# Optimization experiments

Hardware: AMD Instinct MI355X
Metric: run time of the kernel (lower is better)

## Reference

```python
import jax, jax.numpy as jnp
import numpy as np

EPS = 1e-8
TEMP3 = 10.0


def setup_inputs() -> dict:
    key = jax.random.key(0)
    k1, k2, k3 = jax.random.split(key, 3)
    B, D = 8192, 512
    cnn_code = jax.random.normal(k1, (B, D), dtype=jnp.float32)
    rnn_code = jax.random.normal(k2, (B, D), dtype=jnp.float32)
    idx = jax.random.uniform(k3, (B, B), dtype=jnp.float32)
    # ensure every row has at least one positive (> threshold1=0.8), as the
    # original divides by len(pos)
    diag = jnp.arange(B)
    idx = idx.at[diag, diag].set(0.95)
    probs = jnp.array([0.8, 0.5], dtype=jnp.float32)  # (threshold1, threshold2)
    return {"cnn_code": cnn_code, "rnn_code": rnn_code, "idx": idx, "probs": probs}


def reference(cnn_code, rnn_code, idx, probs):
    B = cnn_code.shape[0]
    fdt = cnn_code.dtype
    # cosine similarity * temp3  -> scores0 [B,B]
    cn = jnp.linalg.norm(cnn_code, axis=-1, keepdims=True)   # [B,1]
    rn = jnp.linalg.norm(rnn_code, axis=-1, keepdims=True)   # [B,1]
    scores0 = (cnn_code @ rnn_code.T) / jnp.clip(cn * rn.T, EPS) * TEMP3
    scores1 = scores0.T

    th1, th2 = probs[0], probs[1]
    pos_mask = idx > th1    # [B,B] ragged positive sets per row
    neg_mask = idx <= th2   # [B,B] ragged negative sets per row
    n_pos = pos_mask.sum(axis=1).astype(fdt)          # [B]
    n_neg = neg_mask.sum(axis=1).astype(fdt)          # [B]

    neginf = jnp.array(-jnp.inf, dtype=fdt)
    # logsumexp over each row's negative set (shared across all positives j)
    lse_neg0 = jax.nn.logsumexp(jnp.where(neg_mask, scores0, neginf), axis=1)  # [B]
    lse_neg1 = jax.nn.logsumexp(jnp.where(neg_mask, scores1, neginf), axis=1)  # [B]

    # For each positive j: logits = concat([score_j, neg_scores]); target puts
    # mass 1 on index 0; softXEnt divides by logits length (1 + n_neg).
    denom = (1.0 + n_neg)[:, None]                                            # [B,1]
    l0 = -(scores0 - jnp.logaddexp(scores0, lse_neg0[:, None])) / denom       # [B,B]
    l1 = -(scores1 - jnp.logaddexp(scores1, lse_neg1[:, None])) / denom

    loss0 = (jnp.where(pos_mask, l0, 0.0).sum(axis=1) / n_pos).sum() / B
    loss1 = (jnp.where(pos_mask, l1, 0.0).sum(axis=1) / n_pos).sum() / B
    return loss0 + loss1
```

## Files before the change

kernel.cpp:

```cpp
#include <hip/hip_runtime.h>
#include <hip/hip_bf16.h>
#include <math.h>
#include <stdint.h>

#define BDIM 8192
#define DDIM 512
#define NT   64
#define BK   64
#define TEMP 10.0f
#define PLW  128

typedef __attribute__((ext_vector_type(8))) short bf16x8;
typedef __attribute__((ext_vector_type(4))) float f32x4;
typedef unsigned long long u64;
typedef unsigned int u32;

__device__ __forceinline__ unsigned short f2bf(float f) {
  unsigned int x = __float_as_uint(f);
  x += 0x7fffu + ((x >> 16) & 1u);
  return (unsigned short)(x >> 16);
}

__device__ __forceinline__ void gld16(const void* gptr, void* lptr) {
  __builtin_amdgcn_global_load_lds((const __attribute__((address_space(1))) u32*)gptr,
                                   (__attribute__((address_space(3))) u32*)lptr, 16, 0, 0);
}

__device__ __forceinline__ float red16_dpp(float x) {
  x += __int_as_float(__builtin_amdgcn_mov_dpp(__float_as_int(x), 0xB1, 0xF, 0xF, true));
  x += __int_as_float(__builtin_amdgcn_mov_dpp(__float_as_int(x), 0x4E, 0xF, 0xF, true));
  x += __int_as_float(__builtin_amdgcn_mov_dpp(__float_as_int(x), 0x141, 0xF, 0xF, true));
  x += __int_as_float(__builtin_amdgcn_mov_dpp(__float_as_int(x), 0x140, 0xF, 0xF, true));
  return x;
}

__global__ __launch_bounds__(256) void knorm(const float* __restrict__ cnn,
                                             const float* __restrict__ rnn,
                                             unsigned short* __restrict__ u,
                                             unsigned short* __restrict__ v) {
  int wid = threadIdx.x >> 6, lane = threadIdx.x & 63;
  int gw = blockIdx.x * 4 + wid;
  const float* src;
  unsigned short* dst;
  int row;
  float mul;
  if (gw < BDIM) { src = cnn; dst = u; row = gw; mul = TEMP; }
  else           { src = rnn; dst = v; row = gw - BDIM; mul = 1.0f; }
  const float* p = src + (size_t)row * DDIM + lane * 8;
  float4 a0 = *(const float4*)p;
  float4 a1 = *(const float4*)(p + 4);
  float ss = a0.x*a0.x + a0.y*a0.y + a0.z*a0.z + a0.w*a0.w
           + a1.x*a1.x + a1.y*a1.y + a1.z*a1.z + a1.w*a1.w;
#pragma unroll
  for (int m = 1; m <= 32; m <<= 1) ss += __shfl_xor(ss, m);
  float inv = mul / sqrtf(ss);
  unsigned short o[8];
  o[0] = f2bf(a0.x * inv); o[1] = f2bf(a0.y * inv);
  o[2] = f2bf(a0.z * inv); o[3] = f2bf(a0.w * inv);
  o[4] = f2bf(a1.x * inv); o[5] = f2bf(a1.y * inv);
  o[6] = f2bf(a1.z * inv); o[7] = f2bf(a1.w * inv);
  *(uint4*)(dst + (size_t)row * DDIM + lane * 8) = *(uint4*)o;
}

__global__ __launch_bounds__(256) void kmask(const float* __restrict__ idx,
                                             const float* __restrict__ probs,
                                             unsigned char* __restrict__ posb,
                                             unsigned char* __restrict__ negb,
                                             float* __restrict__ npr,
                                             float* __restrict__ nnr) {
  const float th1 = probs[0], th2 = probs[1];
  int wid = threadIdx.x >> 6, lane = threadIdx.x & 63;
  int row = blockIdx.x * 4 + wid;
  const float4* src = (const float4*)(idx + (size_t)row * BDIM);
  unsigned char* pr = posb + (size_t)row * 1024;
  unsigned char* nr = negb + (size_t)row * 1024;
  int np = 0, nn = 0;
#pragma unroll 2
  for (int i = 0; i < 16; i++) {
    float4 x0 = src[i * 128 + lane * 2];
    float4 x1 = src[i * 128 + lane * 2 + 1];
    float xs[8] = {x0.x, x0.y, x0.z, x0.w, x1.x, x1.y, x1.z, x1.w};
    unsigned pb = 0, nb = 0;
#pragma unroll
    for (int k = 0; k < 8; k++) {
      pb |= (xs[k] > th1 ? 1u : 0u) << k;
      nb |= (xs[k] <= th2 ? 1u : 0u) << k;
    }
    pr[i * 64 + lane] = (unsigned char)pb;
    nr[i * 64 + lane] = (unsigned char)nb;
    np += __popc(pb); nn += __popc(nb);
  }
#pragma unroll
  for (int m = 1; m <= 32; m <<= 1) {
    np += __shfl_xor(np, m);
    nn += __shfl_xor(nn, m);
  }
  if (lane == 0) { npr[row] = (float)np; nnr[row] = (float)nn; }
}

__global__ __launch_bounds__(256, 3) void kmain(const unsigned short* __restrict__ u,
                                                const unsigned short* __restrict__ v,
                                                const u64* __restrict__ posp,
                                                const u64* __restrict__ negp,
                                                float* __restrict__ P) {
  __shared__ unsigned short aT[128 * BK];
  __shared__ unsigned short bT[128 * BK];
  __shared__ float L0[3 * 128];
  __shared__ float L1[3 * 128];
  const int tid = threadIdx.x, lane = tid & 63, wid = tid >> 6;
  const int l15 = lane & 15, lg = lane >> 4;
  const int qr = wid >> 1, qc = wid & 1;

  for (int t = tid; t < 768; t += 256) {
    if (t < 384) L0[t] = 0.f; else L1[t - 384] = 0.f;
  }

  const int bid = blockIdx.x;
  const int xcd = bid & 7, n = bid >> 3;
  const int st = n >> 6, w = n & 63;
  const int ti = xcd * 8 + (w & 7);
  const int tj = st * 8 + (w >> 3);
  const int I = ti * 128, J = tj * 128;

  f32x4 acc[4][4];
#pragma unroll
  for (int a = 0; a < 4; a++)
#pragma unroll
    for (int b = 0; b < 4; b++) acc[a][b] = (f32x4){0, 0, 0, 0};

  const unsigned short* gA = u + (size_t)(I + wid * 32 + (lane >> 3)) * DDIM + (lane & 7) * 8;
  const unsigned short* gB = v + (size_t)(J + wid * 32 + (lane >> 3)) * DDIM + (lane & 7) * 8;
  unsigned short* lA = aT + (wid * 32 + (lane >> 3)) * BK + (lane & 7) * 8;
  unsigned short* lB = bT + (wid * 32 + (lane >> 3)) * BK + (lane & 7) * 8;

  for (int k0 = 0; k0 < DDIM; k0 += BK) {
#pragma unroll
    for (int c = 0; c < 4; c++) {
      gld16(gA + (size_t)c * 8 * DDIM + k0, lA + c * 8 * BK);
      gld16(gB + (size_t)c * 8 * DDIM + k0, lB + c * 8 * BK);
    }
    __syncthreads();
#pragma unroll
    for (int kk = 0; kk < 2; kk++) {
      bf16x8 af[4], bf_[4];
#pragma unroll
      for (int ar = 0; ar < 4; ar++)
        af[ar] = *(const bf16x8*)(aT + (qr * 64 + ar * 16 + l15) * BK + kk * 32 + lg * 8);
#pragma unroll
      for (int bc = 0; bc < 4; bc++)
        bf_[bc] = *(const bf16x8*)(bT + (qc * 64 + bc * 16 + l15) * BK + kk * 32 + lg * 8);
#pragma unroll
      for (int ar = 0; ar < 4; ar++)
#pragma unroll
        for (int bc = 0; bc < 4; bc++)
          acc[ar][bc] = __builtin_amdgcn_mfma_f32_16x16x32_bf16(af[ar], bf_[bc], acc[ar][bc], 0, 0, 0);
    }
    __syncthreads();
  }

  u64 pw1[4], nw1[4];
#pragma unroll
  for (int bc = 0; bc < 4; bc++) {
    size_t w1 = (size_t)(J + qc * 64 + bc * 16 + l15) * PLW + (I >> 6) + qr;
    pw1[bc] = posp[w1] >> (lg * 4);
    nw1[bc] = negp[w1] >> (lg * 4);
  }

  float zn1[4] = {0, 0, 0, 0}, zp1[4] = {0, 0, 0, 0}, sm1[4] = {0, 0, 0, 0};

#pragma unroll
  for (int ar = 0; ar < 4; ar++) {
    u64 pw[4], nw[4];
#pragma unroll
    for (int j = 0; j < 4; j++) {
      int R = qr * 64 + ar * 16 + lg * 4 + j;
      size_t w0 = (size_t)(I + R) * PLW + (J >> 6) + qc;
      pw[j] = posp[w0] >> l15;
      nw[j] = negp[w0] >> l15;
    }
#pragma unroll
    for (int j = 0; j < 4; j++) {
      float zn0 = 0, zp0 = 0, sm0 = 0;
#pragma unroll
      for (int bc = 0; bc < 4; bc++) {
        float s = acc[ar][bc][j];
        float e = __expf(s - TEMP);
        float mp0 = (float)((unsigned)(pw[j]  >> (bc * 16)) & 1u);
        float mn0 = (float)((unsigned)(nw[j]  >> (bc * 16)) & 1u);
        float mp1 = (float)((unsigned)(pw1[bc] >> (ar * 16 + j)) & 1u);
        float mn1 = (float)((unsigned)(nw1[bc] >> (ar * 16 + j)) & 1u);
        zp0 = fmaf(mp0, e, zp0);
        sm0 = fmaf(mp0, s, sm0);
        zn0 = fmaf(mn0, e, zn0);
        zp1[bc] = fmaf(mp1, e, zp1[bc]);
        sm1[bc] = fmaf(mp1, s, sm1[bc]);
        zn1[bc] = fmaf(mn1, e, zn1[bc]);
      }
      zn0 = red16_dpp(zn0); zp0 = red16_dpp(zp0); sm0 = red16_dpp(sm0);
      if (l15 == 0) {
        int R = qr * 64 + ar * 16 + lg * 4 + j;
        atomicAdd(&L0[0 * 128 + R], zn0);
        atomicAdd(&L0[1 * 128 + R], zp0);
        atomicAdd(&L0[2 * 128 + R], sm0);
      }
    }
  }

#pragma unroll
  for (int bc = 0; bc < 4; bc++) {
    float zn = zn1[bc], zp = zp1[bc], sm = sm1[bc];
    zn += __shfl_xor(zn, 16); zn += __shfl_xor(zn, 32);
    zp += __shfl_xor(zp, 16); zp += __shfl_xor(zp, 32);
    sm += __shfl_xor(sm, 16); sm += __shfl_xor(sm, 32);
    if (lg == 0) {
      int C = qc * 64 + bc * 16 + l15;
      atomicAdd(&L1[0 * 128 + C], zn);
      atomicAdd(&L1[1 * 128 + C], zp);
      atomicAdd(&L1[2 * 128 + C], sm);
    }
  }
  __syncthreads();

  for (int t = tid; t < 768; t += 256) {
    int s = t >> 7, c = t & 127;
    if (s < 3) P[((size_t)tj * 6 + s) * BDIM + I + c] = L0[s * 128 + c];
    else       P[((size_t)ti * 6 + s) * BDIM + J + c] = L1[(s - 3) * 128 + c];
  }
}

__global__ __launch_bounds__(128) void kfinal(const float* __restrict__ P,
                                              const float* __restrict__ npr,
                                              const float* __restrict__ nnr,
                                              float* __restrict__ part) {
  int r = blockIdx.x * 128 + threadIdx.x;
  float st[6] = {0, 0, 0, 0, 0, 0};
  for (int k = 0; k < 64; k++) {
#pragma unroll
    for (int s = 0; s < 6; s++) st[s] += P[((size_t)k * 6 + s) * BDIM + r];
  }
  float np = npr[r], nn = nnr[r];
  float inv = 1.f / (np * (1.f + nn));
  float l0 = (np * (TEMP + logf(st[0])) - st[2] + st[1] / st[0]) * inv;
  float l1 = (np * (TEMP + logf(st[3])) - st[5] + st[4] / st[3]) * inv;
  float tot = l0 + l1;
#pragma unroll
  for (int m = 1; m <= 32; m <<= 1) tot += __shfl_xor(tot, m);
  __shared__ float sb;
  if (threadIdx.x == 0) sb = tot;
  __syncthreads();
  if (threadIdx.x == 64) part[blockIdx.x] = sb + tot;
}

__global__ __launch_bounds__(64) void kfinal2(const float* __restrict__ part,
                                              float* __restrict__ out) {
  float t = part[threadIdx.x];
#pragma unroll
  for (int m = 1; m <= 32; m <<= 1) t += __shfl_xor(t, m);
  if (threadIdx.x == 0) out[0] = t / (float)BDIM;
}

extern "C" void kernel_launch(void* const* d_in, const int* in_sizes, int n_in,
                              void* d_out, int out_size, void* d_ws, size_t ws_size,
                              hipStream_t stream) {
  (void)in_sizes; (void)n_in; (void)out_size; (void)ws_size;
  const float* cnn   = (const float*)d_in[0];
  const float* rnn   = (const float*)d_in[1];
  const float* idx   = (const float*)d_in[2];
  const float* probs = (const float*)d_in[3];
  char* w = (char*)d_ws;
  unsigned short* u  = (unsigned short*)w;
  unsigned short* v  = (unsigned short*)(w + 8388608);
  unsigned char* posb = (unsigned char*)(w + 16777216);
  unsigned char* negb = (unsigned char*)(w + 25165824);
  float* P    = (float*)(w + 33554432);
  float* npr  = (float*)(w + 46137344);
  float* nnr  = (float*)(w + 46170112);
  float* part = (float*)(w + 46202880);

  knorm<<<(2 * BDIM) / 4, 256, 0, stream>>>(cnn, rnn, u, v);
  kmask<<<BDIM / 4, 256, 0, stream>>>(idx, probs, posb, negb, npr, nnr);
  kmain<<<NT * NT, 256, 0, stream>>>(u, v, (const u64*)posb, (const u64*)negb, P);
  kfinal<<<BDIM / 128, 128, 0, stream>>>(P, npr, nnr, part);
  kfinal2<<<1, 64, 0, stream>>>(part, (float*)d_out);
}
```

Measured before the change: 223.9 us.

## Fuse mask thresholding into main GEMM kernel and count masks in-tile

Removes the separate mask kernel. Each main-kernel tile now reads its idx block and the transposed idx block, builds positive/negative bitmasks via ballots into shared memory, and accumulates per-row positive/negative counts alongside the other partial sums. This drops one launch and the bitmask round-trip through global memory. In exchange, the full float idx matrix is read twice, and the load latency sits before the GEMM loop.

Measured after the change: 258.4 us. +15.4%, slower.

```diff
diff --git a/kernel.cpp b/kernel.cpp
--- a/kernel.cpp
+++ b/kernel.cpp
@@ -8,7 +8,6 @@
 #define NT   64
 #define BK   64
 #define TEMP 10.0f
-#define PLW  128
 
 typedef __attribute__((ext_vector_type(8))) short bf16x8;
 typedef __attribute__((ext_vector_type(4))) float f32x4;
@@ -62,57 +61,23 @@
   *(uint4*)(dst + (size_t)row * DDIM + lane * 8) = *(uint4*)o;
 }
 
-__global__ __launch_bounds__(256) void kmask(const float* __restrict__ idx,
-                                             const float* __restrict__ probs,
-                                             unsigned char* __restrict__ posb,
-                                             unsigned char* __restrict__ negb,
-                                             float* __restrict__ npr,
-                                             float* __restrict__ nnr) {
-  const float th1 = probs[0], th2 = probs[1];
-  int wid = threadIdx.x >> 6, lane = threadIdx.x & 63;
-  int row = blockIdx.x * 4 + wid;
-  const float4* src = (const float4*)(idx + (size_t)row * BDIM);
-  unsigned char* pr = posb + (size_t)row * 1024;
-  unsigned char* nr = negb + (size_t)row * 1024;
-  int np = 0, nn = 0;
-#pragma unroll 2
-  for (int i = 0; i < 16; i++) {
-    float4 x0 = src[i * 128 + lane * 2];
-    float4 x1 = src[i * 128 + lane * 2 + 1];
-    float xs[8] = {x0.x, x0.y, x0.z, x0.w, x1.x, x1.y, x1.z, x1.w};
-    unsigned pb = 0, nb = 0;
-#pragma unroll
-    for (int k = 0; k < 8; k++) {
-      pb |= (xs[k] > th1 ? 1u : 0u) << k;
-      nb |= (xs[k] <= th2 ? 1u : 0u) << k;
-    }
-    pr[i * 64 + lane] = (unsigned char)pb;
-    nr[i * 64 + lane] = (unsigned char)nb;
-    np += __popc(pb); nn += __popc(nb);
-  }
-#pragma unroll
-  for (int m = 1; m <= 32; m <<= 1) {
-    np += __shfl_xor(np, m);
-    nn += __shfl_xor(nn, m);
-  }
-  if (lane == 0) { npr[row] = (float)np; nnr[row] = (float)nn; }
-}
-
 __global__ __launch_bounds__(256, 3) void kmain(const unsigned short* __restrict__ u,
                                                 const unsigned short* __restrict__ v,
-                                                const u64* __restrict__ posp,
-                                                const u64* __restrict__ negp,
+                                                const float* __restrict__ idx,
+                                                const float* __restrict__ probs,
                                                 float* __restrict__ P) {
   __shared__ unsigned short aT[128 * BK];
   __shared__ unsigned short bT[128 * BK];
-  __shared__ float L0[3 * 128];
+  __shared__ float L0[5 * 128];
   __shared__ float L1[3 * 128];
+  __shared__ u64 m0p[128][2], m0n[128][2];
+  __shared__ u64 m1p[128][2], m1n[128][2];
   const int tid = threadIdx.x, lane = tid & 63, wid = tid >> 6;
   const int l15 = lane & 15, lg = lane >> 4;
   const int qr = wid >> 1, qc = wid & 1;
 
-  for (int t = tid; t < 768; t += 256) {
-    if (t < 384) L0[t] = 0.f; else L1[t - 384] = 0.f;
+  for (int t = tid; t < 1024; t += 256) {
+    if (t < 640) L0[t] = 0.f; else L1[t - 640] = 0.f;
   }
 
   const int bid = blockIdx.x;
@@ -122,6 +87,44 @@
   const int tj = st * 8 + (w >> 3);
   const int I = ti * 128, J = tj * 128;
 
+  const float th1 = probs[0], th2 = probs[1];
+#pragma unroll 1
+  for (int b = 0; b < 8; ++b) {
+    float x[8];
+#pragma unroll
+    for (int t = 0; t < 8; ++t) {
+      int i = b * 8 + t;
+      int r = wid * 32 + (i >> 1), h = i & 1;
+      x[t] = idx[(size_t)(I + r) * BDIM + J + h * 64 + lane];
+    }
+#pragma unroll
+    for (int t = 0; t < 8; ++t) {
+      int i = b * 8 + t;
+      int r = wid * 32 + (i >> 1), h = i & 1;
+      u64 pb = __ballot(x[t] > th1);
+      u64 nb = __ballot(x[t] <= th2);
+      if (lane == 0) { m0p[r][h] = pb; m0n[r][h] = nb; }
+    }
+  }
+#pragma unroll 1
+  for (int b = 0; b < 8; ++b) {
+    float x[8];
+#pragma unroll
+    for (int t = 0; t < 8; ++t) {
+      int i = b * 8 + t;
+      int r = wid * 32 + (i >> 1), h = i & 1;
+      x[t] = idx[(size_t)(J + r) * BDIM + I + h * 64 + lane];
+    }
+#pragma unroll
+    for (int t = 0; t < 8; ++t) {
+      int i = b * 8 + t;
+      int r = wid * 32 + (i >> 1), h = i & 1;
+      u64 pb = __ballot(x[t] > th1);
+      u64 nb = __ballot(x[t] <= th2);
+      if (lane == 0) { m1p[r][h] = pb; m1n[r][h] = nb; }
+    }
+  }
+
   f32x4 acc[4][4];
 #pragma unroll
   for (int a = 0; a < 4; a++)
@@ -161,9 +164,9 @@
   u64 pw1[4], nw1[4];
 #pragma unroll
   for (int bc = 0; bc < 4; bc++) {
-    size_t w1 = (size_t)(J + qc * 64 + bc * 16 + l15) * PLW + (I >> 6) + qr;
-    pw1[bc] = posp[w1] >> (lg * 4);
-    nw1[bc] = negp[w1] >> (lg * 4);
+    int C = qc * 64 + bc * 16 + l15;
+    pw1[bc] = m1p[C][qr] >> (lg * 4);
+    nw1[bc] = m1n[C][qr] >> (lg * 4);
   }
 
   float zn1[4] = {0, 0, 0, 0}, zp1[4] = {0, 0, 0, 0}, sm1[4] = {0, 0, 0, 0};
@@ -174,13 +177,12 @@
 #pragma unroll
     for (int j = 0; j < 4; j++) {
       int R = qr * 64 + ar * 16 + lg * 4 + j;
-      size_t w0 = (size_t)(I + R) * PLW + (J >> 6) + qc;
-      pw[j] = posp[w0] >> l15;
-      nw[j] = negp[w0] >> l15;
+      pw[j] = m0p[R][qc] >> l15;
+      nw[j] = m0n[R][qc] >> l15;
     }
 #pragma unroll
     for (int j = 0; j < 4; j++) {
-      float zn0 = 0, zp0 = 0, sm0 = 0;
+      float zn0 = 0, zp0 = 0, sm0 = 0, cp0 = 0, cn0 = 0;
 #pragma unroll
       for (int bc = 0; bc < 4; bc++) {
         float s = acc[ar][bc][j];
@@ -192,16 +194,21 @@
         zp0 = fmaf(mp0, e, zp0);
         sm0 = fmaf(mp0, s, sm0);
         zn0 = fmaf(mn0, e, zn0);
+        cp0 += mp0;
+        cn0 += mn0;
         zp1[bc] = fmaf(mp1, e, zp1[bc]);
         sm1[bc] = fmaf(mp1, s, sm1[bc]);
         zn1[bc] = fmaf(mn1, e, zn1[bc]);
       }
       zn0 = red16_dpp(zn0); zp0 = red16_dpp(zp0); sm0 = red16_dpp(sm0);
+      cp0 = red16_dpp(cp0); cn0 = red16_dpp(cn0);
       if (l15 == 0) {
         int R = qr * 64 + ar * 16 + lg * 4 + j;
         atomicAdd(&L0[0 * 128 + R], zn0);
         atomicAdd(&L0[1 * 128 + R], zp0);
         atomicAdd(&L0[2 * 128 + R], sm0);
+        atomicAdd(&L0[3 * 128 + R], cp0);
+        atomicAdd(&L0[4 * 128 + R], cn0);
       }
     }
   }
@@ -221,27 +228,25 @@
   }
   __syncthreads();
 
-  for (int t = tid; t < 768; t += 256) {
+  for (int t = tid; t < 1024; t += 256) {
     int s = t >> 7, c = t & 127;
-    if (s < 3) P[((size_t)tj * 6 + s) * BDIM + I + c] = L0[s * 128 + c];
-    else       P[((size_t)ti * 6 + s) * BDIM + J + c] = L1[(s - 3) * 128 + c];
+    if (s < 5) P[((size_t)tj * 8 + s) * BDIM + I + c] = L0[s * 128 + c];
+    else       P[((size_t)ti * 8 + s) * BDIM + J + c] = L1[(s - 5) * 128 + c];
   }
 }
 
 __global__ __launch_bounds__(128) void kfinal(const float* __restrict__ P,
-                                              const float* __restrict__ npr,
-                                              const float* __restrict__ nnr,
                                               float* __restrict__ part) {
   int r = blockIdx.x * 128 + threadIdx.x;
-  float st[6] = {0, 0, 0, 0, 0, 0};
+  float st[8] = {0, 0, 0, 0, 0, 0, 0, 0};
   for (int k = 0; k < 64; k++) {
 #pragma unroll
-    for (int s = 0; s < 6; s++) st[s] += P[((size_t)k * 6 + s) * BDIM + r];
-  }
-  float np = npr[r], nn = nnr[r];
+    for (int s = 0; s < 8; s++) st[s] += P[((size_t)k * 8 + s) * BDIM + r];
+  }
+  float np = st[3], nn = st[4];
   float inv = 1.f / (np * (1.f + nn));
   float l0 = (np * (TEMP + logf(st[0])) - st[2] + st[1] / st[0]) * inv;
-  float l1 = (np * (TEMP + logf(st[3])) - st[5] + st[4] / st[3]) * inv;
+  float l1 = (np * (TEMP + logf(st[5])) - st[7] + st[6] / st[5]) * inv;
   float tot = l0 + l1;
 #pragma unroll
   for (int m = 1; m <= 32; m <<= 1) tot += __shfl_xor(tot, m);
@@ -270,16 +275,11 @@
   char* w = (char*)d_ws;
   unsigned short* u  = (unsigned short*)w;
   unsigned short* v  = (unsigned short*)(w + 8388608);
-  unsigned char* posb = (unsigned char*)(w + 16777216);
-  unsigned char* negb = (unsigned char*)(w + 25165824);
-  float* P    = (float*)(w + 33554432);
-  float* npr  = (float*)(w + 46137344);
-  float* nnr  = (float*)(w + 46170112);
-  float* part = (float*)(w + 46202880);
+  float* P    = (float*)(w + 16777216);
+  float* part = (float*)(w + 33554432);
 
   knorm<<<(2 * BDIM) / 4, 256, 0, stream>>>(cnn, rnn, u, v);
-  kmask<<<BDIM / 4, 256, 0, stream>>>(idx, probs, posb, negb, npr, nnr);
-  kmain<<<NT * NT, 256, 0, stream>>>(u, v, (const u64*)posb, (const u64*)negb, P);
-  kfinal<<<BDIM / 128, 128, 0, stream>>>(P, npr, nnr, part);
+  kmain<<<NT * NT, 256, 0, stream>>>(u, v, idx, probs, P);
+  kfinal<<<BDIM / 128, 128, 0, stream>>>(P, part);
   kfinal2<<<1, 64, 0, stream>>>(part, (float*)d_out);
 }
```
